# Kernel optimization log

Measured on AMD Instinct MI355X. Metric: run time of the kernel, lower is better.

The kernel has to match this reference:

```python
import jax, jax.numpy as jnp
import numpy as np

RES = 2048
STEPS = 65536
SIGMA = 0.01
W = 32  # source computes w from sigma then hardcodes w = 32


def setup_inputs() -> dict:
    key = jax.random.key(0)
    # 3 control points (x, y) in [0, 1]
    control_points = jax.random.uniform(key, (3, 2), dtype=jnp.float32)
    return {"control_points": control_points}


def reference(control_points):
    p0, p1, p2 = control_points[0], control_points[1], control_points[2]
    # lin_interp uses torch.linspace(0, 1, steps)
    t_lin = jnp.linspace(0.0, 1.0, STEPS, dtype=jnp.float32)  # [steps]
    a = p0[:, None] + (p1 - p0)[:, None] * t_lin  # [2, steps]
    b = p1[:, None] + (p2 - p1)[:, None] * t_lin  # [2, steps]
    # forward uses arange(steps)/steps (NOT linspace) for the outer blend
    t_out = jnp.arange(STEPS, dtype=jnp.float32) / float(STEPS)
    curve = a + t_out * (b - a)  # [2, steps]

    # per-step block corner indices (int -> non-differentiable, as in torch .int())
    blocks = jnp.clip(jnp.floor(RES * curve).astype(jnp.int32) - W // 2, 0, RES - W)  # [2, steps]
    bx, by = blocks[0], blocks[1]  # [steps]
    offs = jnp.arange(W, dtype=jnp.int32)

    # grid values inside each block: self.c[a,b,t] = a/res, self.d[a,b,t] = b/res
    ci = (bx[:, None] + offs).astype(jnp.float32) / float(RES)  # [steps, w]
    cj = (by[:, None] + offs).astype(jnp.float32) / float(RES)  # [steps, w]

    dx = curve[0][:, None] - ci  # [steps, w]
    dy = curve[1][:, None] - cj  # [steps, w]
    inv = 1.0 / (2.0 * SIGMA * SIGMA)
    patch = jnp.exp(-(dx[:, :, None] ** 2 + dy[:, None, :] ** 2) * inv)  # [steps, w, w]

    # scatter each step's patch into the grid; mean over steps == sum/steps
    ii = bx[:, None, None] + offs[None, :, None]  # [steps, w, 1] -> broadcast
    jj = by[:, None, None] + offs[None, None, :]  # [steps, 1, w]
    ii = jnp.broadcast_to(ii, (STEPS, W, W))
    jj = jnp.broadcast_to(jj, (STEPS, W, W))
    raster = jnp.zeros((RES, RES), dtype=jnp.float32).at[ii, jj].add(patch)
    return raster / float(STEPS)
```

## Files before the change

### kernel.cpp

```cpp
#include <hip/hip_runtime.h>
#include <hip/hip_bf16.h>

#define RES_    2048
#define CSTEPS  128
#define NWG     512
#define TILE_   48
#define KPAD    136
#define NTHR    576

typedef _Float16 half8 __attribute__((ext_vector_type(8)));
typedef float   float4_ __attribute__((ext_vector_type(4)));
typedef int     int4_   __attribute__((ext_vector_type(4)));

__global__ __launch_bounds__(1024) void zero_out(float4_* __restrict__ out) {
    out[(size_t)blockIdx.x * 1024 + threadIdx.x] = float4_{0.f, 0.f, 0.f, 0.f};
}

__global__ __launch_bounds__(NTHR) void bezier_scatter(const float* __restrict__ cp,
                                                       float* __restrict__ out) {
    __shared__ _Float16 sExT[TILE_][KPAD];
    __shared__ _Float16 sEyT[TILE_][KPAD];
    __shared__ float s_cx[CSTEPS], s_cy[CSTEPS];
    __shared__ int   s_bx[CSTEPS], s_by[CSTEPS];
    __shared__ int   s_Ax, s_Ay;

    const int tid = threadIdx.x;

    if (tid < CSTEPS) {
        const int gs = blockIdx.x * CSTEPS + tid;
        const float tl = (float)((double)gs / 65535.0);
        const float to = (float)gs * (1.0f / 65536.0f);
        const float p0x = cp[0], p0y = cp[1], p1x = cp[2], p1y = cp[3], p2x = cp[4], p2y = cp[5];
        const float ax = __fadd_rn(p0x, __fmul_rn(__fsub_rn(p1x, p0x), tl));
        const float ay = __fadd_rn(p0y, __fmul_rn(__fsub_rn(p1y, p0y), tl));
        const float bxf = __fadd_rn(p1x, __fmul_rn(__fsub_rn(p2x, p1x), tl));
        const float byf = __fadd_rn(p1y, __fmul_rn(__fsub_rn(p2y, p1y), tl));
        const float cx = __fadd_rn(ax, __fmul_rn(to, __fsub_rn(bxf, ax)));
        const float cy = __fadd_rn(ay, __fmul_rn(to, __fsub_rn(byf, ay)));
        const int bxi = min(max((int)floorf(__fmul_rn(2048.0f, cx)) - 16, 0), RES_ - 32);
        const int byi = min(max((int)floorf(__fmul_rn(2048.0f, cy)) - 16, 0), RES_ - 32);
        s_cx[tid] = cx; s_cy[tid] = cy; s_bx[tid] = bxi; s_by[tid] = byi;
        if (tid == 0) {
            s_Ax = min(max(bxi - 8, 0), RES_ - TILE_);
            s_Ay = min(max(byi - 8, 0), RES_ - TILE_);
        }
    }
    __syncthreads();
    const int Ax = s_Ax, Ay = s_Ay;

    for (int it = tid; it < 2 * TILE_ * (CSTEPS / 8); it += NTHR) {
        const int half_ = TILE_ * (CSTEPS / 8);
        const int table = (it >= half_);
        const int rem   = it - table * half_;
        const int o     = rem >> 4;
        const int s0    = (rem & 15) * 8;
        const float* cc = table ? s_cy : s_cx;
        const int*   bb = table ? s_by : s_bx;
        const int  base = table ? Ay : Ax;
        const float ci  = (float)(base + o) * (1.0f / 2048.0f);
        const float4_ cA = *(const float4_*)&cc[s0];
        const float4_ cB = *(const float4_*)&cc[s0 + 4];
        const int4_   bA = *(const int4_*)&bb[s0];
        const int4_   bB = *(const int4_*)&bb[s0 + 4];
        half8 v;
        #pragma unroll
        for (int j = 0; j < 8; ++j) {
            const float cs = (j < 4) ? cA[j & 3] : cB[j & 3];
            const int   bs = (j < 4) ? bA[j & 3] : bB[j & 3];
            const float d = __fsub_rn(cs, ci);
            const float e = __expf(-__fmul_rn(__fmul_rn(d, d), 5000.0f));
            const unsigned orel = (unsigned)(base + o - bs);
            v[j] = (orel < 32u) ? (_Float16)e : (_Float16)0.0f;
        }
        *(half8*)(table ? &sEyT[o][s0] : &sExT[o][s0]) = v;
    }
    __syncthreads();

    const int lane = tid & 63;
    const int wid  = tid >> 6;
    const int mt   = wid / 3, nt = wid - mt * 3;
    const int arow = mt * 16 + (lane & 15);
    const int bcol = nt * 16 + (lane & 15);
    const int kgrp = (lane >> 4) * 8;
    float4_ acc = {0.f, 0.f, 0.f, 0.f};
    #pragma unroll
    for (int kb = 0; kb < CSTEPS / 32; ++kb) {
        const half8 aF = *(const half8*)&sExT[arow][kb * 32 + kgrp];
        const half8 bF = *(const half8*)&sEyT[bcol][kb * 32 + kgrp];
        acc = __builtin_amdgcn_mfma_f32_16x16x32_f16(aF, bF, acc, 0, 0, 0);
    }

    const int coll = lane & 15;
    const int rowb = (lane >> 4) * 4;
    #pragma unroll
    for (int r = 0; r < 4; ++r) {
        const float v = acc[r];
        if (v != 0.0f) {
            const int gx = Ax + mt * 16 + rowb + r;
            const int gy = Ay + nt * 16 + coll;
            atomicAdd(&out[gx * RES_ + gy], v * (1.0f / 65536.0f));
        }
    }
}

extern "C" void kernel_launch(void* const* d_in, const int* in_sizes, int n_in,
                              void* d_out, int out_size, void* d_ws, size_t ws_size,
                              hipStream_t stream) {
    const float* cp = (const float*)d_in[0];
    float* out = (float*)d_out;
    hipLaunchKernelGGL(zero_out, dim3(1024), dim3(1024), 0, stream, (float4_*)out);
    hipLaunchKernelGGL(bezier_scatter, dim3(NWG), dim3(NTHR), 0, stream, cp, out);
}
```

Measured before the change: 21.04 us.

## Fold output zeroing into compute kernel and defer atomics to flush kernel

The separate zeroing kernel is removed. Each compute workgroup now zeroes its own 32 KB slice of the output, while the patch computation runs at the same time. Per-workgroup 48x48 tile results are written to workspace along with their anchor corners. A second kernel then performs the atomic adds into the output. This hides the zeroing cost behind the MFMA work and keeps atomics out of the compute kernel, at the price of workspace traffic and a kernel boundary that is still needed to order zeroing before the atomics.

```diff
diff --git a/kernel.cpp b/kernel.cpp
--- a/kernel.cpp
+++ b/kernel.cpp
@@ -7,17 +7,16 @@
 #define TILE_   48
 #define KPAD    136
 #define NTHR    576
+#define WSTILE  2304
 
 typedef _Float16 half8 __attribute__((ext_vector_type(8)));
 typedef float   float4_ __attribute__((ext_vector_type(4)));
 typedef int     int4_   __attribute__((ext_vector_type(4)));
 
-__global__ __launch_bounds__(1024) void zero_out(float4_* __restrict__ out) {
-    out[(size_t)blockIdx.x * 1024 + threadIdx.x] = float4_{0.f, 0.f, 0.f, 0.f};
-}
-
-__global__ __launch_bounds__(NTHR) void bezier_scatter(const float* __restrict__ cp,
-                                                       float* __restrict__ out) {
+__global__ __launch_bounds__(NTHR) void bezier_stage(const float* __restrict__ cp,
+                                                     float* __restrict__ out,
+                                                     float* __restrict__ wst,
+                                                     int* __restrict__ wsa) {
     __shared__ _Float16 sExT[TILE_][KPAD];
     __shared__ _Float16 sEyT[TILE_][KPAD];
     __shared__ float s_cx[CSTEPS], s_cy[CSTEPS];
@@ -25,9 +24,17 @@
     __shared__ int   s_Ax, s_Ay;
 
     const int tid = threadIdx.x;
+    const int bid = blockIdx.x;
+
+    {
+        float4_* oz = (float4_*)out + (size_t)bid * 2048;
+        #pragma unroll
+        for (int i = tid; i < 2048; i += NTHR)
+            oz[i] = float4_{0.f, 0.f, 0.f, 0.f};
+    }
 
     if (tid < CSTEPS) {
-        const int gs = blockIdx.x * CSTEPS + tid;
+        const int gs = bid * CSTEPS + tid;
         const float tl = (float)((double)gs / 65535.0);
         const float to = (float)gs * (1.0f / 65536.0f);
         const float p0x = cp[0], p0y = cp[1], p1x = cp[2], p1y = cp[3], p2x = cp[4], p2y = cp[5];
@@ -43,6 +50,8 @@
         if (tid == 0) {
             s_Ax = min(max(bxi - 8, 0), RES_ - TILE_);
             s_Ay = min(max(byi - 8, 0), RES_ - TILE_);
+            wsa[2 * bid]     = s_Ax;
+            wsa[2 * bid + 1] = s_Ay;
         }
     }
     __syncthreads();
@@ -90,17 +99,28 @@
         acc = __builtin_amdgcn_mfma_f32_16x16x32_f16(aF, bF, acc, 0, 0, 0);
     }
 
+    float* wt = wst + (size_t)bid * WSTILE;
     const int coll = lane & 15;
     const int rowb = (lane >> 4) * 4;
     #pragma unroll
-    for (int r = 0; r < 4; ++r) {
-        const float v = acc[r];
-        if (v != 0.0f) {
-            const int gx = Ax + mt * 16 + rowb + r;
-            const int gy = Ay + nt * 16 + coll;
-            atomicAdd(&out[gx * RES_ + gy], v * (1.0f / 65536.0f));
-        }
-    }
+    for (int r = 0; r < 4; ++r)
+        wt[(mt * 16 + rowb + r) * TILE_ + nt * 16 + coll] = acc[r] * (1.0f / 65536.0f);
+}
+
+__global__ __launch_bounds__(NTHR) void bezier_flush(const float* __restrict__ wst,
+                                                     const int* __restrict__ wsa,
+                                                     float* __restrict__ out) {
+    const int tid = threadIdx.x;
+    const int bid = blockIdx.x;
+    const int Ax = wsa[2 * bid], Ay = wsa[2 * bid + 1];
+    const int idx = tid * 4;
+    const int row = idx / TILE_;
+    const int col = idx - row * TILE_;
+    const float4_ v = *(const float4_*)&wst[(size_t)bid * WSTILE + idx];
+    float* orow = &out[(size_t)(Ax + row) * RES_ + Ay + col];
+    #pragma unroll
+    for (int i = 0; i < 4; ++i)
+        if (v[i] != 0.0f) atomicAdd(&orow[i], v[i]);
 }
 
 extern "C" void kernel_launch(void* const* d_in, const int* in_sizes, int n_in,
@@ -108,6 +128,9 @@
                               hipStream_t stream) {
     const float* cp = (const float*)d_in[0];
     float* out = (float*)d_out;
-    hipLaunchKernelGGL(zero_out, dim3(1024), dim3(1024), 0, stream, (float4_*)out);
-    hipLaunchKernelGGL(bezier_scatter, dim3(NWG), dim3(NTHR), 0, stream, cp, out);
+    float* wst = (float*)d_ws;
+    int*   wsa = (int*)((char*)d_ws + (size_t)NWG * WSTILE * 4);
+
+    hipLaunchKernelGGL(bezier_stage, dim3(NWG), dim3(NTHR), 0, stream, cp, out, wst, wsa);
+    hipLaunchKernelGGL(bezier_flush, dim3(NWG), dim3(NTHR), 0, stream, wst, wsa, out);
 }
```

After: 31.50 us. +49.7%, slower.
